# Performance work log

Hardware: AMD Instinct MI355X
Metric: run time of the kernel (lower is better)

The kernel has to match this reference:

```python
import jax, jax.numpy as jnp
import numpy as np

HIS = 10   # history steps (node_feature_dim = 10*4)
ROLL = 2   # args.pred_roll
MP = 2     # message_passing_steps
N = 20000  # num nodes (balls)
E = 320000 # num edges


def _mlp(x, W1, b1, W2, b2, g, be):
    # two-layer ELU MLP + BatchNorm1d (training mode: batch statistics)
    h = jax.nn.elu(x @ W1 + b1)
    h = jax.nn.elu(h @ W2 + b2)
    B, M, C = h.shape
    f = h.reshape(B * M, C)
    mu = f.mean(0)
    var = ((f - mu) ** 2).mean(0)  # biased variance, as torch BN training
    f = (f - mu) * jax.lax.rsqrt(var + 1e-5) * g + be
    return f.reshape(B, M, C)


def setup_inputs() -> dict:
    key = jax.random.key(0)
    ks = jax.random.split(key, 16)

    def lin(k, i, o):
        W = jax.random.normal(k, (i, o), jnp.float32) / jnp.sqrt(jnp.float32(i))
        b = jnp.full((o,), 0.1, jnp.float32)
        return W, b

    inp = {}
    inp["nodes"] = jax.random.normal(ks[0], (1, HIS + ROLL, N, 4), jnp.float32)
    inp["edge_pair"] = jax.random.randint(ks[1], (E, 2), 0, N)
    inp["edge_attr"] = jax.random.normal(ks[2], (E, 2), jnp.float32)
    # encoder node MLP: 40 -> 128 -> 128
    inp["en_W1"], inp["en_b1"] = lin(ks[3], 40, 128)
    inp["en_W2"], inp["en_b2"] = lin(ks[4], 128, 128)
    inp["en_g"], inp["en_be"] = jnp.ones((128,), jnp.float32), jnp.zeros((128,), jnp.float32)
    # encoder edge MLP: 6 -> 32 -> 32
    inp["ee_W1"], inp["ee_b1"] = lin(ks[5], 6, 32)
    inp["ee_W2"], inp["ee_b2"] = lin(ks[6], 32, 32)
    inp["ee_g"], inp["ee_be"] = jnp.ones((32,), jnp.float32), jnp.zeros((32,), jnp.float32)
    # GraphNetBlock edge MLP: 288 -> 128 -> 32
    inp["ge_W1"], inp["ge_b1"] = lin(ks[7], 288, 128)
    inp["ge_W2"], inp["ge_b2"] = lin(ks[8], 128, 32)
    inp["ge_g"], inp["ge_be"] = jnp.ones((32,), jnp.float32), jnp.zeros((32,), jnp.float32)
    # GraphNetBlock node MLP: 160 -> 256 -> 128
    inp["gn_W1"], inp["gn_b1"] = lin(ks[9], 160, 256)
    inp["gn_W2"], inp["gn_b2"] = lin(ks[10], 256, 128)
    inp["gn_g"], inp["gn_be"] = jnp.ones((128,), jnp.float32), jnp.zeros((128,), jnp.float32)
    # decoder: Linear(128,128) Tanh Linear(128,2)
    inp["d_W1"], inp["d_b1"] = lin(ks[11], 128, 128)
    inp["d_W2"], inp["d_b2"] = lin(ks[12], 128, 2)
    return inp


def _forward(nodes, edge_pair, edge_attr,
             en_W1, en_b1, en_W2, en_b2, en_g, en_be,
             ee_W1, ee_b1, ee_W2, ee_b2, ee_g, ee_be,
             ge_W1, ge_b1, ge_W2, ge_b2, ge_g, ge_be,
             gn_W1, gn_b1, gn_W2, gn_b2, gn_g, gn_be,
             d_W1, d_b1, d_W2, d_b2):
    window = nodes[0]                 # [T, N, 4]
    n = window.shape[1]
    s0 = edge_pair[:, 0]
    s1 = edge_pair[:, 1]
    # history features: [1, N, HIS*4]
    history = jnp.transpose(window[:HIS], (1, 0, 2)).reshape(1, n, -1)
    gt_future = window[HIS:]          # [ROLL, N, 4]
    # initial edge features: raw 2-dim attr + |pos/vel diff| (4-dim) -> 6
    pd0 = jnp.abs(window[HIS][s0] - window[HIS][s1])   # [E, 4]
    edge_feat = jnp.concatenate([edge_attr[None], pd0[None]], -1)  # [1, E, 6]
    cur_pos = window[HIS - 1, :, :2]
    cur_vel = window[HIS - 1, :, 2:]
    preds = []
    for _ in range(ROLL):
        ln = _mlp(history, en_W1, en_b1, en_W2, en_b2, en_g, en_be)    # [1,N,128]
        le = _mlp(edge_feat, ee_W1, ee_b1, ee_W2, ee_b2, ee_g, ee_be)  # [1,E,32]
        for _ in range(MP):
            # edge update: gather sender/receiver, MLP
            ef = jnp.concatenate([ln[:, s0], ln[:, s1], le], -1)       # [1,E,288]
            ne = _mlp(ef, ge_W1, ge_b1, ge_W2, ge_b2, ge_g, ge_be)     # [1,E,32]
            # node aggregation: scatter-add at both endpoints
            agg = jnp.zeros((n, ne.shape[-1]), ne.dtype)
            agg = agg.at[s0].add(ne[0]).at[s1].add(ne[0])
            nf = jnp.concatenate([ln, agg[None]], -1)                  # [1,N,160]
            nn_ = _mlp(nf, gn_W1, gn_b1, gn_W2, gn_b2, gn_g, gn_be)
            ln = nn_ + ln
            le = ne + le
        accel = jnp.tanh(ln @ d_W1 + d_b1) @ d_W2 + d_b2               # [1,N,2]
        prev_pos = cur_pos
        cur_pos = 2 * cur_pos + accel - prev_pos                       # [1,N,2]
        cur_vel = cur_vel + accel
        pd = jnp.abs(cur_pos[:, s0] - cur_pos[:, s1])                  # [1,E,2]
        edge_feat = edge_feat.at[:, :, -2:].set(pd)
        preds.append(cur_pos)
        hist4 = history.reshape(1, n, HIS, 4)
        new_state = jnp.concatenate([cur_pos.reshape(1, n, 1, 2),
                                     cur_vel.reshape(1, n, 1, 2)], -1)
        history = jnp.concatenate([hist4[:, :, 1:, :], new_state], -2).reshape(1, n, -1)
    preds = jnp.stack(preds, 1)                                        # [1,ROLL,N,2]
    diff = preds[0] - gt_future[:, :, :2]
    variance = 5e-5
    loss_nll = (diff ** 2 / (2 * variance)).sum() / (ROLL * n)
    loss_mse = (diff ** 2).mean()
    return preds, loss_nll, loss_mse, gt_future


def reference(nodes, edge_pair, edge_attr,
              en_W1, en_b1, en_W2, en_b2, en_g, en_be,
              ee_W1, ee_b1, ee_W2, ee_b2, ee_g, ee_be,
              ge_W1, ge_b1, ge_W2, ge_b2, ge_g, ge_be,
              gn_W1, gn_b1, gn_W2, gn_b2, gn_g, gn_be,
              d_W1, d_b1, d_W2, d_b2):
    return _forward(nodes, edge_pair, edge_attr,
                    en_W1, en_b1, en_W2, en_b2, en_g, en_be,
                    ee_W1, ee_b1, ee_W2, ee_b2, ee_g, ee_be,
                    ge_W1, ge_b1, ge_W2, ge_b2, ge_g, ge_be,
                    gn_W1, gn_b1, gn_W2, gn_b2, gn_g, gn_be,
                    d_W1, d_b1, d_W2, d_b2)
```

## Files before the change

kernel.cpp:

```cpp
#include <hip/hip_runtime.h>


constexpr int NN = 20000;
constexpr int NE = 320000;
constexpr int NSLOT = 32;
constexpr int SSTR = 512;

typedef __attribute__((ext_vector_type(8))) short short8;
typedef __attribute__((ext_vector_type(4))) float f32x4;

__device__ __forceinline__ float act_elu(float x) { return x > 0.f ? x : __expf(x) - 1.f; }
__device__ __forceinline__ unsigned short f2bf(float f) {
  unsigned u = __builtin_bit_cast(unsigned, f);
  return (unsigned short)((u + 0x7FFFu + ((u >> 16) & 1u)) >> 16);
}
__device__ __forceinline__ float bf2f(unsigned short h) {
  unsigned u = ((unsigned)h) << 16; return __builtin_bit_cast(float, u);
}

template<int K1, int K1P, int C1, int C2, int BM, int NWM, int NWC, int NWM2, int NWC2,
         int ACT2, bool STATS, int MODE>
__global__ __launch_bounds__(256) void mlp2_k(
    const unsigned short* __restrict__ A, const unsigned short* __restrict__ A2,
    const unsigned short* __restrict__ Wt1, const float* __restrict__ b1,
    const unsigned short* __restrict__ Wt2, const float* __restrict__ b2,
    unsigned short* __restrict__ out, int M, float* __restrict__ stat)
{
  constexpr int FM  = BM / (16 * NWM);
  constexpr int FC  = C1 / (16 * NWC);
  constexpr int FM2 = BM / (16 * NWM2);
  constexpr int FC2 = C2 / (16 * NWC2);
  constexpr int NKS1 = K1P / 32;
  constexpr int NKS2 = C1 / 32;
  constexpr int AST = K1P + 8;
  constexpr int P1 = C1 + 8;
  constexpr int P2 = C2 + 8;
  constexpr int ACH = K1P / 8;
  static_assert(NWM * NWC == 4 && NWM2 * NWC2 == 4, "4 waves");
  static_assert(C2 <= C1, "repack reuses H1");

  __shared__ unsigned short As[BM * AST];
  __shared__ unsigned short H1[BM * P1];
  __shared__ float red[2][C2];

  const int tid = threadIdx.x;
  const int row0 = blockIdx.x * BM;
  const int wave = tid >> 6, lane = tid & 63;
  const int wm = wave % NWM, wc = wave / NWM;
  const int wm2 = wave % NWM2, wc2 = wave / NWM2;
  const int lr = lane & 15, kg = lane >> 4;

  if (STATS) for (int i = tid; i < 2 * C2; i += 256) ((float*)red)[i] = 0.f;

  for (int idx = tid; idx < BM * ACH; idx += 256) {
    int m = idx / ACH, chk = idx % ACH;
    int kglob = chk * 8;
    int row = row0 + m;
    uint4 v = make_uint4(0, 0, 0, 0);
    if (row < M) {
      if (MODE == 0) {
        if (kglob + 8 <= K1) v = *(const uint4*)(A + (size_t)row * K1 + kglob);
      } else if (MODE == 2) {
        v = (kglob < 128) ? *(const uint4*)(A + (size_t)row * 128 + kglob)
                          : *(const uint4*)(A2 + (size_t)row * 32 + (kglob - 128));
      } else {
        if (chk == 0) v = *(const uint4*)(A + (size_t)row * 8);
      }
    }
    *(uint4*)&As[m * AST + chk * 8] = v;
  }
  __syncthreads();

  f32x4 acc1[FM][FC];
#pragma unroll
  for (int i = 0; i < FM; ++i)
#pragma unroll
    for (int j = 0; j < FC; ++j) acc1[i][j] = (f32x4){0.f, 0.f, 0.f, 0.f};

#pragma unroll
  for (int ks = 0; ks < NKS1; ++ks) {
    const int k0 = ks * 32;
    short8 af[FM], bfr[FC];
#pragma unroll
    for (int i = 0; i < FM; ++i) {
      int r = (wm * FM + i) * 16 + lr;
      af[i] = __builtin_bit_cast(short8, *(const uint4*)&As[r * AST + k0 + kg * 8]);
    }
#pragma unroll
    for (int j = 0; j < FC; ++j) {
      int c = (wc * FC + j) * 16 + lr;
      bfr[j] = __builtin_bit_cast(short8, *(const uint4*)&Wt1[(size_t)c * K1P + k0 + kg * 8]);
    }
#pragma unroll
    for (int i = 0; i < FM; ++i)
#pragma unroll
      for (int j = 0; j < FC; ++j)
        acc1[i][j] = __builtin_amdgcn_mfma_f32_16x16x32_bf16(af[i], bfr[j], acc1[i][j], 0, 0, 0);
  }

  {
    float bl1[FC];
#pragma unroll
    for (int j = 0; j < FC; ++j) bl1[j] = b1[(wc * FC + j) * 16 + lr];
#pragma unroll
    for (int i = 0; i < FM; ++i)
#pragma unroll
      for (int t = 0; t < 4; ++t) {
        int rl = (wm * FM + i) * 16 + kg * 4 + t;
#pragma unroll
        for (int j = 0; j < FC; ++j)
          H1[rl * P1 + (wc * FC + j) * 16 + lr] = f2bf(act_elu(acc1[i][j][t] + bl1[j]));
      }
  }
  __syncthreads();

  f32x4 acc2[FM2][FC2];
#pragma unroll
  for (int i = 0; i < FM2; ++i)
#pragma unroll
    for (int j = 0; j < FC2; ++j) acc2[i][j] = (f32x4){0.f, 0.f, 0.f, 0.f};

#pragma unroll
  for (int ks = 0; ks < NKS2; ++ks) {
    const int k0 = ks * 32;
    short8 af[FM2], bfr[FC2];
#pragma unroll
    for (int i = 0; i < FM2; ++i) {
      int r = (wm2 * FM2 + i) * 16 + lr;
      af[i] = __builtin_bit_cast(short8, *(const uint4*)&H1[r * P1 + k0 + kg * 8]);
    }
#pragma unroll
    for (int j = 0; j < FC2; ++j) {
      int c = (wc2 * FC2 + j) * 16 + lr;
      bfr[j] = __builtin_bit_cast(short8, *(const uint4*)&Wt2[(size_t)c * C1 + k0 + kg * 8]);
    }
#pragma unroll
    for (int i = 0; i < FM2; ++i)
#pragma unroll
      for (int j = 0; j < FC2; ++j)
        acc2[i][j] = __builtin_amdgcn_mfma_f32_16x16x32_bf16(af[i], bfr[j], acc2[i][j], 0, 0, 0);
  }
  __syncthreads();

  float psum[FC2], psq[FC2], bl2[FC2];
#pragma unroll
  for (int j = 0; j < FC2; ++j) {
    psum[j] = 0.f; psq[j] = 0.f;
    bl2[j] = b2[(wc2 * FC2 + j) * 16 + lr];
  }
#pragma unroll
  for (int i = 0; i < FM2; ++i)
#pragma unroll
    for (int t = 0; t < 4; ++t) {
      int rl = (wm2 * FM2 + i) * 16 + kg * 4 + t;
      bool ok = (row0 + rl) < M;
#pragma unroll
      for (int j = 0; j < FC2; ++j) {
        float v = acc2[i][j][t] + bl2[j];
        if (ACT2 == 1) v = act_elu(v);
        else if (ACT2 == 2) v = tanhf(v);
        if (STATS && ok) { psum[j] += v; psq[j] += v * v; }
        H1[rl * P2 + (wc2 * FC2 + j) * 16 + lr] = f2bf(v);
      }
    }
  if (STATS) {
#pragma unroll
    for (int j = 0; j < FC2; ++j) {
      int c = (wc2 * FC2 + j) * 16 + lr;
      atomicAdd(&red[0][c], psum[j]);
      atomicAdd(&red[1][c], psq[j]);
    }
  }
  __syncthreads();
  for (int idx = tid; idx < BM * (C2 / 8); idx += 256) {
    int r = idx / (C2 / 8), cc = idx % (C2 / 8);
    int row = row0 + r;
    if (row < M)
      *(uint4*)&out[(size_t)row * C2 + cc * 8] = *(const uint4*)&H1[r * P2 + cc * 8];
  }
  if (STATS) {
    float* st = stat + (size_t)(blockIdx.x & (NSLOT - 1)) * SSTR;
    for (int i = tid; i < C2; i += 256) {
      atomicAdd(&st[i], red[0][i]);
      atomicAdd(&st[256 + i], red[1][i]);
    }
  }
}

template<int K, int C, int BM, int NWM, int NWC, int ACT>
__global__ __launch_bounds__(256) void mgemm_k(
    const unsigned short* __restrict__ A,
    const unsigned short* __restrict__ Wt, const float* __restrict__ bias,
    unsigned short* __restrict__ out, int M)
{
  constexpr int FM = BM / (16 * NWM);
  constexpr int FC = C / (16 * NWC);
  constexpr int NKS = K / 32;
  constexpr int AST = K + 8;
  constexpr int P2 = C + 8;
  constexpr int ACH = K / 8;
  static_assert(NWM * NWC == 4, "4 waves");

  __shared__ unsigned short As[BM * AST];
  __shared__ unsigned short Ob[BM * P2];

  const int tid = threadIdx.x;
  const int row0 = blockIdx.x * BM;
  const int wave = tid >> 6, lane = tid & 63;
  const int wm = wave % NWM, wc = wave / NWM;
  const int lr = lane & 15, kg = lane >> 4;

  for (int idx = tid; idx < BM * ACH; idx += 256) {
    int m = idx / ACH, chk = idx % ACH;
    int row = row0 + m;
    uint4 v = make_uint4(0, 0, 0, 0);
    if (row < M) v = *(const uint4*)(A + (size_t)row * K + chk * 8);
    *(uint4*)&As[m * AST + chk * 8] = v;
  }
  __syncthreads();

  f32x4 acc[FM][FC];
#pragma unroll
  for (int i = 0; i < FM; ++i)
#pragma unroll
    for (int j = 0; j < FC; ++j) acc[i][j] = (f32x4){0.f, 0.f, 0.f, 0.f};

#pragma unroll
  for (int ks = 0; ks < NKS; ++ks) {
    const int k0 = ks * 32;
    short8 af[FM], bfr[FC];
#pragma unroll
    for (int i = 0; i < FM; ++i) {
      int r = (wm * FM + i) * 16 + lr;
      af[i] = __builtin_bit_cast(short8, *(const uint4*)&As[r * AST + k0 + kg * 8]);
    }
#pragma unroll
    for (int j = 0; j < FC; ++j) {
      int c = (wc * FC + j) * 16 + lr;
      bfr[j] = __builtin_bit_cast(short8, *(const uint4*)&Wt[(size_t)c * K + k0 + kg * 8]);
    }
#pragma unroll
    for (int i = 0; i < FM; ++i)
#pragma unroll
      for (int j = 0; j < FC; ++j)
        acc[i][j] = __builtin_amdgcn_mfma_f32_16x16x32_bf16(af[i], bfr[j], acc[i][j], 0, 0, 0);
  }

  float bl[FC];
#pragma unroll
  for (int j = 0; j < FC; ++j) bl[j] = bias[(wc * FC + j) * 16 + lr];
#pragma unroll
  for (int i = 0; i < FM; ++i)
#pragma unroll
    for (int t = 0; t < 4; ++t) {
      int rl = (wm * FM + i) * 16 + kg * 4 + t;
#pragma unroll
      for (int j = 0; j < FC; ++j) {
        float v = acc[i][j][t] + bl[j];
        if (ACT == 1) v = act_elu(v);
        else if (ACT == 2) v = tanhf(v);
        Ob[rl * P2 + (wc * FC + j) * 16 + lr] = f2bf(v);
      }
    }
  __syncthreads();
  for (int idx = tid; idx < BM * (C / 8); idx += 256) {
    int r = idx / (C / 8), cc = idx % (C / 8);
    int row = row0 + r;
    if (row < M)
      *(uint4*)&out[(size_t)row * C + cc * 8] = *(const uint4*)&Ob[r * P2 + cc * 8];
  }
}

template<int WOUT>
__global__ __launch_bounds__(256) void ge_edge_k(
    const unsigned short* __restrict__ Pb,
    const unsigned short* __restrict__ leb,
    const int* __restrict__ epP,
    const unsigned short* __restrict__ Wt1c,
    const float* __restrict__ b1,
    const unsigned short* __restrict__ Wt2,
    const float* __restrict__ b2,
    unsigned short* __restrict__ out,
    float* __restrict__ aggF,
    float* __restrict__ stat)
{
  constexpr int BM = 64;
  constexpr int P1 = 136;
  __shared__ unsigned short Ps[BM * P1];
  __shared__ unsigned short As[BM * 40];
  __shared__ float red[2][32];
  __shared__ int eps[BM * 2];

  const int tid = threadIdx.x;
  const int e0 = blockIdx.x * BM;
  const int wave = tid >> 6, lane = tid & 63;
  const int lr = lane & 15, kg = lane >> 4;
  const int wm = wave & 1, wc = wave >> 1;

  uint4 g0[4], g1[4];
  int gm[4], gch[4];
#pragma unroll
  for (int t = 0; t < 4; ++t) {
    int idx = tid + 256 * t;
    int m = idx >> 4, ch = idx & 15;
    gm[t] = m; gch[t] = ch;
    int s0 = epP[2 * (e0 + m)];
    int s1 = epP[2 * (e0 + m) + 1];
    g0[t] = *(const uint4*)&Pb[(size_t)s0 * 256 + ch * 8];
    g1[t] = *(const uint4*)&Pb[(size_t)s1 * 256 + 128 + ch * 8];
  }

  if (tid < BM * 2) eps[tid] = epP[e0 * 2 + tid];
  {
    int m = tid >> 2, chk = tid & 3;
    *(uint4*)&As[m * 40 + chk * 8] = *(const uint4*)&leb[(size_t)(e0 + m) * 32 + chk * 8];
  }
  short8 wf1[4];
#pragma unroll
  for (int j = 0; j < 4; ++j)
    wf1[j] = __builtin_bit_cast(short8, *(const uint4*)&Wt1c[(size_t)((wc * 4 + j) * 16 + lr) * 32 + kg * 8]);
  if (tid < 64) ((float*)red)[tid] = 0.f;
  __syncthreads();

  f32x4 acc1[2][4];
#pragma unroll
  for (int i = 0; i < 2; ++i)
#pragma unroll
    for (int j = 0; j < 4; ++j) acc1[i][j] = (f32x4){0.f, 0.f, 0.f, 0.f};
  {
    short8 af[2];
#pragma unroll
    for (int i = 0; i < 2; ++i)
      af[i] = __builtin_bit_cast(short8, *(const uint4*)&As[((wm * 2 + i) * 16 + lr) * 40 + kg * 8]);
#pragma unroll
    for (int i = 0; i < 2; ++i)
#pragma unroll
      for (int j = 0; j < 4; ++j)
        acc1[i][j] = __builtin_amdgcn_mfma_f32_16x16x32_bf16(af[i], wf1[j], acc1[i][j], 0, 0, 0);
  }

#pragma unroll
  for (int t = 0; t < 4; ++t) {
    uint4 o;
    const unsigned short* ap = (const unsigned short*)&g0[t];
    const unsigned short* bp = (const unsigned short*)&g1[t];
    unsigned short* op = (unsigned short*)&o;
#pragma unroll
    for (int j = 0; j < 8; ++j) op[j] = f2bf(bf2f(ap[j]) + bf2f(bp[j]));
    *(uint4*)&Ps[gm[t] * P1 + gch[t] * 8] = o;
  }
  __syncthreads();

  {
    float bl1[4];
#pragma unroll
    for (int j = 0; j < 4; ++j) bl1[j] = b1[(wc * 4 + j) * 16 + lr];
#pragma unroll
    for (int i = 0; i < 2; ++i)
#pragma unroll
      for (int t = 0; t < 4; ++t) {
        int rl = (wm * 2 + i) * 16 + kg * 4 + t;
#pragma unroll
        for (int j = 0; j < 4; ++j) {
          int a = rl * P1 + (wc * 4 + j) * 16 + lr;
          Ps[a] = f2bf(act_elu(acc1[i][j][t] + bl1[j] + bf2f(Ps[a])));
        }
      }
  }
  __syncthreads();

  f32x4 acc2[2];
  acc2[0] = (f32x4){0.f, 0.f, 0.f, 0.f};
  acc2[1] = (f32x4){0.f, 0.f, 0.f, 0.f};
  const int r2 = wave * 16 + lr;
#pragma unroll
  for (int ks = 0; ks < 4; ++ks) {
    int k0 = ks * 32;
    short8 a2 = __builtin_bit_cast(short8, *(const uint4*)&Ps[r2 * P1 + k0 + kg * 8]);
#pragma unroll
    for (int j = 0; j < 2; ++j) {
      short8 b2f = __builtin_bit_cast(short8, *(const uint4*)&Wt2[(size_t)(j * 16 + lr) * 128 + k0 + kg * 8]);
      acc2[j] = __builtin_amdgcn_mfma_f32_16x16x32_bf16(a2, b2f, acc2[j], 0, 0, 0);
    }
  }

  float psum[2] = {0.f, 0.f}, psq[2] = {0.f, 0.f};
  float bl2[2] = {b2[lr], b2[16 + lr]};
#pragma unroll
  for (int t = 0; t < 4; ++t) {
    int rl = wave * 16 + kg * 4 + t;
#pragma unroll
    for (int j = 0; j < 2; ++j) {
      float v = act_elu(acc2[j][t] + bl2[j]);
      psum[j] += v; psq[j] += v * v;
      As[rl * 40 + j * 16 + lr] = f2bf(v);
    }
  }
#pragma unroll
  for (int j = 0; j < 2; ++j) {
    atomicAdd(&red[0][j * 16 + lr], psum[j]);
    atomicAdd(&red[1][j * 16 + lr], psq[j]);
  }
  __syncthreads();
  if (WOUT) {
    int m = tid >> 2, chk = tid & 3;
    *(uint4*)&out[(size_t)(e0 + m) * 32 + chk * 8] = *(const uint4*)&As[m * 40 + chk * 8];
  }
  {
    int c = tid & 31, gsel = tid >> 5;
    int rbeg = gsel * 8;
    float acc = 0.f;
    int cur = eps[2 * rbeg];
#pragma unroll
    for (int r = 0; r < 8; ++r) {
      int row = rbeg + r;
      float v = bf2f(As[row * 40 + c]);
      int s0 = eps[2 * row];
      if (s0 != cur) { atomicAdd(&aggF[(size_t)cur * 32 + c], acc); acc = 0.f; cur = s0; }
      acc += v;
      atomicAdd(&aggF[(size_t)eps[2 * row + 1] * 32 + c], v);
    }
    atomicAdd(&aggF[(size_t)cur * 32 + c], acc);
  }
  if (tid < 32) {
    float* st = stat + (size_t)(blockIdx.x & (NSLOT - 1)) * SSTR;
    atomicAdd(&st[tid], red[0][tid]);
    atomicAdd(&st[256 + tid], red[1][tid]);
  }
}

__global__ __launch_bounds__(256) void agg_fin_k(float* __restrict__ aggF,
    const float* __restrict__ stat, float invM,
    const float* __restrict__ g, const float* __restrict__ be,
    const int* __restrict__ deg0, const int* __restrict__ deg1,
    unsigned short* __restrict__ agg_bf, int N)
{
  __shared__ float s_scl[32], s_shf[32];
  if (threadIdx.x < 32) {
    int c = threadIdx.x;
    float su = 0.f, sq = 0.f;
    for (int s = 0; s < NSLOT; ++s) {
      su += stat[(size_t)s * SSTR + c];
      sq += stat[(size_t)s * SSTR + 256 + c];
    }
    float mu = su * invM;
    float var = sq * invM - mu * mu;
    float sc = rsqrtf(var + 1e-5f) * g[c];
    s_scl[c] = sc; s_shf[c] = be[c] - mu * sc;
  }
  __syncthreads();
  int i = blockIdx.x * 256 + threadIdx.x;
  if (i >= N * 32) return;
  int n = i >> 5, c = i & 31;
  float v = fmaf(s_scl[c], aggF[i], (float)(deg0[n] + deg1[n]) * s_shf[c]);
  agg_bf[i] = f2bf(v);
  aggF[i] = 0.f;
}

__global__ __launch_bounds__(256) void wtrans_all_k(
    const float* __restrict__ enW1, const float* __restrict__ enW2,
    const float* __restrict__ geW1, const float* __restrict__ geW2,
    const float* __restrict__ gnW1, const float* __restrict__ gnW2,
    const float* __restrict__ dW1,  const float* __restrict__ eeW1,
    const float* __restrict__ eeW2,
    unsigned short* __restrict__ enW1t, unsigned short* __restrict__ enW2t,
    unsigned short* __restrict__ gePt,  unsigned short* __restrict__ geCt,
    unsigned short* __restrict__ geW2t,
    unsigned short* __restrict__ gnW1t, unsigned short* __restrict__ gnW2t,
    unsigned short* __restrict__ dW1t,  unsigned short* __restrict__ eeW1t,
    unsigned short* __restrict__ eeW2t)
{
  int i = blockIdx.x * 256 + threadIdx.x;
#define SEG(Wsrc, Wdst, NROW, SRCS, KS, KP) \
  { int n = (NROW) * (KP); \
    if (i < n) { int c = i / (KP), k = i - c * (KP); \
      (Wdst)[i] = (k < (KS)) ? f2bf((Wsrc)[(size_t)k * (SRCS) + c]) : (unsigned short)0; return; } \
    i -= n; }
  SEG(enW1, enW1t, 128, 128, 40, 64)
  SEG(enW2, enW2t, 128, 128, 128, 128)
  SEG(geW1, gePt, 128, 128, 128, 128)
  SEG(geW1 + 128 * 128, gePt + 128 * 128, 128, 128, 128, 128)
  SEG(geW1 + 256 * 128, geCt, 128, 128, 32, 32)
  SEG(geW2, geW2t, 32, 32, 128, 128)
  SEG(gnW1, gnW1t, 256, 256, 160, 160)
  SEG(gnW2, gnW2t, 128, 128, 256, 256)
  SEG(dW1,  dW1t,  128, 128, 128, 128)
  SEG(eeW1, eeW1t, 32, 32, 6, 32)
  SEG(eeW2, eeW2t, 32, 32, 32, 32)
#undef SEG
}
constexpr int WT_TOTAL = 128*64 + 128*128 + 128*128 + 128*128 + 128*32 + 32*128
                       + 256*160 + 128*256 + 128*128 + 32*32 + 32*32;

template<int C, bool RES>
__global__ __launch_bounds__(256) void normb_k(const unsigned short* __restrict__ h,
    const float* __restrict__ stat, float invM,
    const float* __restrict__ g, const float* __restrict__ be,
    unsigned short* __restrict__ out_bf, int total8)
{
  __shared__ float s_scl[C], s_shf[C];
  for (int i = threadIdx.x; i < C; i += 256) {
    float su = 0.f, sq = 0.f;
    for (int s = 0; s < NSLOT; ++s) {
      su += stat[(size_t)s * SSTR + i];
      sq += stat[(size_t)s * SSTR + 256 + i];
    }
    float mu = su * invM;
    float var = sq * invM - mu * mu;
    float sc = rsqrtf(var + 1e-5f) * g[i];
    s_scl[i] = sc; s_shf[i] = be[i] - mu * sc;
  }
  __syncthreads();
  int i = blockIdx.x * 256 + threadIdx.x;
  if (i >= total8) return;
  int c8 = (i % (C / 8)) * 8;
  uint4 hv = ((const uint4*)h)[i];
  const unsigned short* hp = (const unsigned short*)&hv;
  float f[8];
#pragma unroll
  for (int j = 0; j < 8; ++j) f[j] = fmaf(bf2f(hp[j]), s_scl[c8 + j], s_shf[c8 + j]);
  if (RES) {
    uint4 pv = ((const uint4*)out_bf)[i];
    const unsigned short* pp = (const unsigned short*)&pv;
#pragma unroll
    for (int j = 0; j < 8; ++j) f[j] += bf2f(pp[j]);
  }
  uint4 o;
  unsigned short* op = (unsigned short*)&o;
#pragma unroll
  for (int j = 0; j < 8; ++j) op[j] = f2bf(f[j]);
  ((uint4*)out_bf)[i] = o;
}

__global__ __launch_bounds__(256) void csr_count0_k(const int* __restrict__ ep,
    int* __restrict__ deg0, int E)
{
  int e = blockIdx.x * 256 + threadIdx.x;
  if (e < E) atomicAdd(&deg0[ep[2 * e]], 1);
}

__global__ __launch_bounds__(1024) void csr_scan_k(const int* __restrict__ deg,
    int* __restrict__ off, int* __restrict__ cursor, int N)
{
  __shared__ int part[1024];
  int t = threadIdx.x;
  const int CHK = (N + 1023) / 1024;
  int c0 = t * CHK, c1 = min(c0 + CHK, N);
  int s = 0;
  for (int i = c0; i < c1; ++i) s += deg[i];
  part[t] = s;
  __syncthreads();
  for (int o = 1; o < 1024; o <<= 1) {
    int v = (t >= o) ? part[t - o] : 0;
    __syncthreads();
    part[t] += v;
    __syncthreads();
  }
  int run = t ? part[t - 1] : 0;
  for (int i = c0; i < c1; ++i) { int d = deg[i]; off[i] = run; cursor[i] = run; run += d; }
}

__global__ __launch_bounds__(256) void csr_fill0_k(const int* __restrict__ ep,
    int* __restrict__ cursor0, int* __restrict__ perm, int E)
{
  int e = blockIdx.x * 256 + threadIdx.x;
  if (e < E) { int p = atomicAdd(&cursor0[ep[2 * e]], 1); perm[p] = e; }
}

__global__ __launch_bounds__(256) void permute_edges_k(const float4* __restrict__ nodes4,
    const float* __restrict__ attr, const int* __restrict__ ep,
    const int* __restrict__ perm, int* __restrict__ epP,
    unsigned short* __restrict__ efb, int* __restrict__ deg1, int E)
{
  int e2 = blockIdx.x * 256 + threadIdx.x;
  if (e2 >= E) return;
  int e = perm[e2];
  int s0 = ep[2 * e], s1 = ep[2 * e + 1];
  epP[2 * e2] = s0; epP[2 * e2 + 1] = s1;
  atomicAdd(&deg1[s1], 1);
  float4 w0 = nodes4[(size_t)10 * NN + s0];
  float4 w1 = nodes4[(size_t)10 * NN + s1];
  float2 a = ((const float2*)attr)[e];
  uint4 o;
  o.x = (unsigned)f2bf(a.x) | ((unsigned)f2bf(a.y) << 16);
  o.y = (unsigned)f2bf(fabsf(w0.x - w1.x)) | ((unsigned)f2bf(fabsf(w0.y - w1.y)) << 16);
  o.z = (unsigned)f2bf(fabsf(w0.z - w1.z)) | ((unsigned)f2bf(fabsf(w0.w - w1.w)) << 16);
  o.w = 0;
  ((uint4*)efb)[e2] = o;
}

__global__ __launch_bounds__(256) void le_upd_k(const unsigned short* __restrict__ h2e,
    const float* __restrict__ stat, float invM,
    const float* __restrict__ g, const float* __restrict__ be,
    unsigned short* __restrict__ leb, int total8)
{
  __shared__ float s_scl[32], s_shf[32];
  if (threadIdx.x < 32) {
    int c = threadIdx.x;
    float su = 0.f, sq = 0.f;
    for (int s = 0; s < NSLOT; ++s) {
      su += stat[(size_t)s * SSTR + c];
      sq += stat[(size_t)s * SSTR + 256 + c];
    }
    float mu = su * invM;
    float var = sq * invM - mu * mu;
    float sc = rsqrtf(var + 1e-5f) * g[c];
    s_scl[c] = sc; s_shf[c] = be[c] - mu * sc;
  }
  __syncthreads();
  int i = blockIdx.x * 256 + threadIdx.x;
  if (i >= total8) return;
  int c8 = (i & 3) * 8;
  uint4 hv = ((const uint4*)h2e)[i];
  uint4 lv = ((const uint4*)leb)[i];
  const unsigned short* hp = (const unsigned short*)&hv;
  const unsigned short* lp = (const unsigned short*)&lv;
  uint4 o;
  unsigned short* op = (unsigned short*)&o;
#pragma unroll
  for (int j = 0; j < 8; ++j)
    op[j] = f2bf(bf2f(lp[j]) + fmaf(bf2f(hp[j]), s_scl[c8 + j], s_shf[c8 + j]));
  ((uint4*)leb)[i] = o;
}

__global__ __launch_bounds__(256) void dec2i_k(const unsigned short* __restrict__ T,
    const float* __restrict__ W2, const float* __restrict__ b2,
    float* __restrict__ pos, float* __restrict__ vel, float* __restrict__ preds, int M)
{
  __shared__ float Wl[256];
  Wl[threadIdx.x] = W2[threadIdx.x];
  __syncthreads();
  int row = blockIdx.x * 256 + threadIdx.x;
  if (row >= M) return;
  float ax = b2[0], ay = b2[1];
  const uint4* t4 = (const uint4*)(T + (size_t)row * 128);
#pragma unroll
  for (int k8 = 0; k8 < 16; ++k8) {
    uint4 v = t4[k8];
    const unsigned short* p = (const unsigned short*)&v;
#pragma unroll
    for (int j = 0; j < 8; ++j) {
      float f = bf2f(p[j]);
      int k = k8 * 8 + j;
      ax = fmaf(f, Wl[2 * k], ax);
      ay = fmaf(f, Wl[2 * k + 1], ay);
    }
  }
  float2 p = ((float2*)pos)[row], vv = ((float2*)vel)[row];
  p.x += ax; p.y += ay; vv.x += ax; vv.y += ay;
  ((float2*)pos)[row] = p; ((float2*)vel)[row] = vv;
  ((float2*)preds)[row] = p;
}

__global__ __launch_bounds__(256) void pd_upd_k(const float* __restrict__ pos,
    const int* __restrict__ epP, unsigned short* __restrict__ efb, int E)
{
  int e = blockIdx.x * 256 + threadIdx.x;
  if (e >= E) return;
  float2 p0 = ((const float2*)pos)[epP[2 * e]];
  float2 p1 = ((const float2*)pos)[epP[2 * e + 1]];
  unsigned u = (unsigned)f2bf(fabsf(p0.x - p1.x)) | ((unsigned)f2bf(fabsf(p0.y - p1.y)) << 16);
  *(unsigned*)&efb[(size_t)e * 8 + 4] = u;
}

__global__ __launch_bounds__(256) void hist_shift_k(float* __restrict__ hist,
    unsigned short* __restrict__ histb,
    const float* __restrict__ pos, const float* __restrict__ vel, int M)
{
  int n = blockIdx.x * 256 + threadIdx.x;
  if (n >= M) return;
  float4* h4 = (float4*)(hist + (size_t)n * 40);
  float4 tmp[10];
#pragma unroll
  for (int t = 0; t < 10; ++t) tmp[t] = h4[t];
  float2 pp = ((const float2*)pos)[n], vv = ((const float2*)vel)[n];
  unsigned* hb = (unsigned*)(histb + (size_t)n * 40);
#pragma unroll
  for (int t = 0; t < 9; ++t) {
    float4 v = tmp[t + 1];
    h4[t] = v;
    hb[2 * t]     = (unsigned)f2bf(v.x) | ((unsigned)f2bf(v.y) << 16);
    hb[2 * t + 1] = (unsigned)f2bf(v.z) | ((unsigned)f2bf(v.w) << 16);
  }
  float4 nv = make_float4(pp.x, pp.y, vv.x, vv.y);
  h4[9] = nv;
  hb[18] = (unsigned)f2bf(nv.x) | ((unsigned)f2bf(nv.y) << 16);
  hb[19] = (unsigned)f2bf(nv.z) | ((unsigned)f2bf(nv.w) << 16);
}

__global__ __launch_bounds__(256) void init_nodes_k(const float4* __restrict__ nodes4,
    float* __restrict__ hist, unsigned short* __restrict__ histb,
    float* __restrict__ pos, float* __restrict__ vel,
    float* __restrict__ outGt, int M)
{
  int n = blockIdx.x * 256 + threadIdx.x;
  if (n >= M) return;
  float4* h4 = (float4*)(hist + (size_t)n * 40);
  unsigned* hb = (unsigned*)(histb + (size_t)n * 40);
  float4 v;
#pragma unroll
  for (int t = 0; t < 10; ++t) {
    v = nodes4[(size_t)t * M + n];
    h4[t] = v;
    hb[2 * t]     = (unsigned)f2bf(v.x) | ((unsigned)f2bf(v.y) << 16);
    hb[2 * t + 1] = (unsigned)f2bf(v.z) | ((unsigned)f2bf(v.w) << 16);
  }
  ((float2*)pos)[n] = make_float2(v.x, v.y);
  ((float2*)vel)[n] = make_float2(v.z, v.w);
  float4 g0 = nodes4[(size_t)10 * M + n];
  float4 g1 = nodes4[(size_t)11 * M + n];
  float2* gt2 = (float2*)outGt;
  gt2[(size_t)2 * n + 0] = make_float2(g0.x, g0.y);
  gt2[(size_t)2 * n + 1] = make_float2(g0.z, g0.w);
  gt2[(size_t)2 * (M + n) + 0] = make_float2(g1.x, g1.y);
  gt2[(size_t)2 * (M + n) + 1] = make_float2(g1.z, g1.w);
}

__global__ __launch_bounds__(256) void loss_k(const float* __restrict__ preds,
    const float* __restrict__ gtf, float* __restrict__ acc)
{
  int i = blockIdx.x * 256 + threadIdx.x;
  float d2 = 0.f;
  if (i < 2 * NN * 2) {
    int r = i / (NN * 2);
    int rem = i - r * (NN * 2);
    int n = rem >> 1, c = rem & 1;
    float df = preds[i] - gtf[((size_t)r * NN + n) * 4 + c];
    d2 = df * df;
  }
#pragma unroll
  for (int o = 32; o > 0; o >>= 1) d2 += __shfl_down(d2, o, 64);
  __shared__ float sb[4];
  int lane = threadIdx.x & 63, w = threadIdx.x >> 6;
  if (lane == 0) sb[w] = d2;
  __syncthreads();
  if (threadIdx.x == 0) atomicAdd(acc, sb[0] + sb[1] + sb[2] + sb[3]);
}

__global__ void loss_write_k(const float* __restrict__ acc, float* __restrict__ o)
{
  float s = *acc;
  o[0] = s * 0.25f;
  o[1] = s * (1.f / 80000.f);
}

extern "C" void kernel_launch(void* const* d_in, const int* in_sizes, int n_in,
                              void* d_out, int out_size, void* d_ws, size_t ws_size,
                              hipStream_t stream)
{
  (void)in_sizes; (void)n_in; (void)out_size; (void)ws_size;
  const float* nodes = (const float*)d_in[0];
  const int*   ep    = (const int*)d_in[1];
  const float* eattr = (const float*)d_in[2];
  const float *en_W1 = (const float*)d_in[3],  *en_b1 = (const float*)d_in[4],
              *en_W2 = (const float*)d_in[5],  *en_b2 = (const float*)d_in[6],
              *en_g  = (const float*)d_in[7],  *en_be = (const float*)d_in[8];
  const float *ee_W1 = (const float*)d_in[9],  *ee_b1 = (const float*)d_in[10],
              *ee_W2 = (const float*)d_in[11], *ee_b2 = (const float*)d_in[12],
              *ee_g  = (const float*)d_in[13], *ee_be = (const float*)d_in[14];
  const float *ge_W1 = (const float*)d_in[15], *ge_b1 = (const float*)d_in[16],
              *ge_W2 = (const float*)d_in[17], *ge_b2 = (const float*)d_in[18],
              *ge_g  = (const float*)d_in[19], *ge_be = (const float*)d_in[20];
  const float *gn_W1 = (const float*)d_in[21], *gn_b1 = (const float*)d_in[22],
              *gn_W2 = (const float*)d_in[23], *gn_b2 = (const float*)d_in[24],
              *gn_g  = (const float*)d_in[25], *gn_be = (const float*)d_in[26];
  const float *d_W1  = (const float*)d_in[27], *d_b1  = (const float*)d_in[28],
              *d_W2  = (const float*)d_in[29], *d_b2  = (const float*)d_in[30];

  float* out = (float*)d_out;
  float* outPreds = out;
  float* outLoss  = out + 80000;
  float* outGt    = out + 80002;

  float* ws = (float*)d_ws;
  size_t off = 0;
  auto alloc = [&](size_t nf) { float* p = ws + off; off += (nf + 15) & ~(size_t)15; return p; };
  float* hist  = alloc((size_t)NN * 40);
  unsigned short* histb = (unsigned short*)alloc((size_t)NN * 20);
  unsigned short* efb   = (unsigned short*)alloc((size_t)NE * 4);
  unsigned short* lnb  = (unsigned short*)alloc((size_t)NN * 64);
  unsigned short* leb  = (unsigned short*)alloc((size_t)NE * 16);
  unsigned short* e32b = (unsigned short*)alloc((size_t)NE * 16);
  unsigned short* Pb   = (unsigned short*)alloc((size_t)NN * 128);
  unsigned short* h2nb = (unsigned short*)alloc((size_t)NN * 64);
  unsigned short* dtb  = (unsigned short*)alloc((size_t)NN * 64);
  unsigned short* aggb = (unsigned short*)alloc((size_t)NN * 16);
  float* aggF  = alloc((size_t)NN * 32);
  float* pos   = alloc((size_t)NN * 2);
  float* vel   = alloc((size_t)NN * 2);
  unsigned short* enW1t = (unsigned short*)alloc(128 * 64 / 2);
  unsigned short* enW2t = (unsigned short*)alloc(128 * 128 / 2);
  unsigned short* gePt  = (unsigned short*)alloc(256 * 128 / 2);
  unsigned short* geCt  = (unsigned short*)alloc(128 * 32 / 2);
  unsigned short* geW2t = (unsigned short*)alloc(32 * 128 / 2);
  unsigned short* gnW1t = (unsigned short*)alloc(256 * 160 / 2);
  unsigned short* gnW2t = (unsigned short*)alloc(128 * 256 / 2);
  unsigned short* dW1t  = (unsigned short*)alloc(128 * 128 / 2);
  unsigned short* eeW1t = (unsigned short*)alloc(32 * 32 / 2);
  unsigned short* eeW2t = (unsigned short*)alloc(32 * 32 / 2);
  const size_t SLOTSZ = (size_t)NSLOT * SSTR;
  float* statArr = alloc(12 * SLOTSZ + 256 + 16);
  float* zerosF  = statArr + 12 * SLOTSZ;
  float* lacc    = zerosF + 256;
  int* deg0    = (int*)alloc(NN);
  int* off0    = (int*)alloc(NN);
  int* cursor0 = (int*)alloc(NN);
  int* deg1    = (int*)alloc(NN);
  int* perm    = (int*)alloc(NE);
  int* epP     = (int*)alloc(2 * (size_t)NE);

  hipMemsetAsync(statArr, 0, (12 * SLOTSZ + 256 + 16) * sizeof(float), stream);
  hipMemsetAsync(deg0, 0, NN * sizeof(int), stream);
  hipMemsetAsync(deg1, 0, NN * sizeof(int), stream);
  hipMemsetAsync(aggF, 0, (size_t)NN * 32 * sizeof(float), stream);

  wtrans_all_k<<<(WT_TOTAL + 255) / 256, 256, 0, stream>>>(
      en_W1, en_W2, ge_W1, ge_W2, gn_W1, gn_W2, d_W1, ee_W1, ee_W2,
      enW1t, enW2t, gePt, geCt, geW2t, gnW1t, gnW2t, dW1t, eeW1t, eeW2t);

  init_nodes_k<<<(NN + 255) / 256, 256, 0, stream>>>((const float4*)nodes, hist, histb, pos, vel, outGt, NN);

  csr_count0_k<<<(NE + 255) / 256, 256, 0, stream>>>(ep, deg0, NE);
  csr_scan_k<<<1, 1024, 0, stream>>>(deg0, off0, cursor0, NN);
  csr_fill0_k<<<(NE + 255) / 256, 256, 0, stream>>>(ep, cursor0, perm, NE);
  permute_edges_k<<<(NE + 255) / 256, 256, 0, stream>>>(
      (const float4*)nodes, eattr, ep, perm, epP, efb, deg1, NE);

  const int GN32 = (NN + 31) / 32;
  const int GE128 = NE / 128;
  const int GE64 = NE / 64;
  const int G_N8 = (NN * 16 + 255) / 256;
  const int G_E8 = (NE * 4 + 255) / 256;
  const int G_AGG = (NN * 32 + 255) / 256;

  for (int r = 0; r < 2; ++r) {
    float* sEN = statArr + (size_t)(r * 6 + 0) * SLOTSZ;
    float* sEE = statArr + (size_t)(r * 6 + 1) * SLOTSZ;

    mlp2_k<40, 64, 128, 128, 32, 2, 2, 2, 2, 1, true, 0><<<GN32, 256, 0, stream>>>(
        histb, nullptr, enW1t, en_b1, enW2t, en_b2, h2nb, NN, sEN);
    normb_k<128, false><<<G_N8, 256, 0, stream>>>(h2nb, sEN, 1.f / NN, en_g, en_be, lnb, NN * 16);

    mlp2_k<32, 32, 32, 32, 128, 4, 1, 4, 1, 1, true, 3><<<GE128, 256, 0, stream>>>(
        efb, nullptr, eeW1t, ee_b1, eeW2t, ee_b2, e32b, NE, sEE);
    normb_k<32, false><<<G_E8, 256, 0, stream>>>(e32b, sEE, 1.f / NE, ee_g, ee_be, leb, NE * 4);

    for (int mp = 0; mp < 2; ++mp) {
      float* sGE = statArr + (size_t)(r * 6 + 2 + mp * 2) * SLOTSZ;
      float* sGN = statArr + (size_t)(r * 6 + 3 + mp * 2) * SLOTSZ;

      mgemm_k<128, 256, 32, 2, 2, 0><<<GN32, 256, 0, stream>>>(lnb, gePt, zerosF, Pb, NN);
      if (mp == 0)
        ge_edge_k<1><<<GE64, 256, 0, stream>>>(Pb, leb, epP, geCt, ge_b1, geW2t, ge_b2, e32b, aggF, sGE);
      else
        ge_edge_k<0><<<GE64, 256, 0, stream>>>(Pb, leb, epP, geCt, ge_b1, geW2t, ge_b2, e32b, aggF, sGE);

      agg_fin_k<<<G_AGG, 256, 0, stream>>>(aggF, sGE, 1.f / NE, ge_g, ge_be, deg0, deg1, aggb, NN);
      if (mp == 0)
        le_upd_k<<<G_E8, 256, 0, stream>>>(e32b, sGE, 1.f / NE, ge_g, ge_be, leb, NE * 4);

      mlp2_k<160, 160, 256, 128, 32, 2, 2, 2, 2, 1, true, 2><<<GN32, 256, 0, stream>>>(
          lnb, aggb, gnW1t, gn_b1, gnW2t, gn_b2, h2nb, NN, sGN);
      normb_k<128, true><<<G_N8, 256, 0, stream>>>(h2nb, sGN, 1.f / NN, gn_g, gn_be, lnb, NN * 16);
    }

    mgemm_k<128, 128, 32, 2, 2, 2><<<GN32, 256, 0, stream>>>(lnb, dW1t, d_b1, dtb, NN);
    dec2i_k<<<(NN + 255) / 256, 256, 0, stream>>>(dtb, d_W2, d_b2, pos, vel, outPreds + (size_t)r * NN * 2, NN);

    if (r == 0) {
      pd_upd_k<<<(NE + 255) / 256, 256, 0, stream>>>(pos, epP, efb, NE);
      hist_shift_k<<<(NN + 255) / 256, 256, 0, stream>>>(hist, histb, pos, vel, NN);
    }
  }

  loss_k<<<(2 * NN * 2 + 255) / 256, 256, 0, stream>>>(outPreds, outGt, lacc);
  loss_write_k<<<1, 1, 0, stream>>>(lacc, outLoss);
}
```

Baseline: 789.7 us.

## Fuse BN finalize, edge residual update and decoder head into neighboring kernels

```diff
diff --git a/kernel.cpp b/kernel.cpp
--- a/kernel.cpp
+++ b/kernel.cpp
@@ -21,10 +21,13 @@
 template<int K1, int K1P, int C1, int C2, int BM, int NWM, int NWC, int NWM2, int NWC2,
          int ACT2, bool STATS, int MODE>
 __global__ __launch_bounds__(256) void mlp2_k(
-    const unsigned short* __restrict__ A, const unsigned short* __restrict__ A2,
+    const unsigned short* __restrict__ A,
     const unsigned short* __restrict__ Wt1, const float* __restrict__ b1,
     const unsigned short* __restrict__ Wt2, const float* __restrict__ b2,
-    unsigned short* __restrict__ out, int M, float* __restrict__ stat)
+    unsigned short* __restrict__ out, int M, float* __restrict__ stat,
+    float* __restrict__ aggF, const float* __restrict__ statP, float invE,
+    const float* __restrict__ gg, const float* __restrict__ gb,
+    float* __restrict__ sclW, const int* __restrict__ dg0, const int* __restrict__ dg1)
 {
   constexpr int FM  = BM / (16 * NWM);
   constexpr int FC  = C1 / (16 * NWC);
@@ -42,6 +45,7 @@
   __shared__ unsigned short As[BM * AST];
   __shared__ unsigned short H1[BM * P1];
   __shared__ float red[2][C2];
+  __shared__ float s_scl[(MODE == 4) ? 32 : 1], s_shf[(MODE == 4) ? 32 : 1];
 
   const int tid = threadIdx.x;
   const int row0 = blockIdx.x * BM;
@@ -52,19 +56,49 @@
 
   if (STATS) for (int i = tid; i < 2 * C2; i += 256) ((float*)red)[i] = 0.f;
 
+  if constexpr (MODE == 4) {
+    if (tid < 32) {
+      float su = 0.f, sq = 0.f;
+      for (int s = 0; s < NSLOT; ++s) {
+        su += statP[(size_t)s * SSTR + tid];
+        sq += statP[(size_t)s * SSTR + 256 + tid];
+      }
+      float mu = su * invE;
+      float var = sq * invE - mu * mu;
+      float sc = rsqrtf(var + 1e-5f) * gg[tid];
+      float sh = gb[tid] - mu * sc;
+      s_scl[tid] = sc; s_shf[tid] = sh;
+      if (blockIdx.x == 0) { sclW[tid] = sc; sclW[32 + tid] = sh; }
+    }
+    __syncthreads();
+  }
+
   for (int idx = tid; idx < BM * ACH; idx += 256) {
     int m = idx / ACH, chk = idx % ACH;
     int kglob = chk * 8;
     int row = row0 + m;
     uint4 v = make_uint4(0, 0, 0, 0);
     if (row < M) {
-      if (MODE == 0) {
+      if constexpr (MODE == 0) {
         if (kglob + 8 <= K1) v = *(const uint4*)(A + (size_t)row * K1 + kglob);
-      } else if (MODE == 2) {
-        v = (kglob < 128) ? *(const uint4*)(A + (size_t)row * 128 + kglob)
-                          : *(const uint4*)(A2 + (size_t)row * 32 + (kglob - 128));
+      } else if constexpr (MODE == 3) {
+        if (chk == 0) v = *(const uint4*)(A + (size_t)row * 8);
       } else {
-        if (chk == 0) v = *(const uint4*)(A + (size_t)row * 8);
+        if (kglob < 128) {
+          v = *(const uint4*)(A + (size_t)row * 128 + kglob);
+        } else {
+          int c0 = kglob - 128;
+          float* ap = &aggF[(size_t)row * 32 + c0];
+          float4 a0 = *(float4*)ap, a1 = *(float4*)(ap + 4);
+          *(float4*)ap = make_float4(0.f, 0.f, 0.f, 0.f);
+          *(float4*)(ap + 4) = make_float4(0.f, 0.f, 0.f, 0.f);
+          float d = (float)(dg0[row] + dg1[row]);
+          float av[8] = {a0.x, a0.y, a0.z, a0.w, a1.x, a1.y, a1.z, a1.w};
+          unsigned short* vp = (unsigned short*)&v;
+#pragma unroll
+          for (int j = 0; j < 8; ++j)
+            vp[j] = f2bf(fmaf(s_scl[c0 + j], av[j], d * s_shf[c0 + j]));
+        }
       }
     }
     *(uint4*)&As[m * AST + chk * 8] = v;
@@ -187,11 +221,13 @@
   }
 }
 
-template<int K, int C, int BM, int NWM, int NWC, int ACT>
+template<int K, int C, int BM, int NWM, int NWC, int ACT, int DEC>
 __global__ __launch_bounds__(256) void mgemm_k(
     const unsigned short* __restrict__ A,
     const unsigned short* __restrict__ Wt, const float* __restrict__ bias,
-    unsigned short* __restrict__ out, int M)
+    unsigned short* __restrict__ out, int M,
+    const float* __restrict__ W2f, const float* __restrict__ b2f,
+    float* __restrict__ pos, float* __restrict__ vel, float* __restrict__ preds)
 {
   constexpr int FM = BM / (16 * NWM);
   constexpr int FC = C / (16 * NWC);
@@ -203,6 +239,7 @@
 
   __shared__ unsigned short As[BM * AST];
   __shared__ unsigned short Ob[BM * P2];
+  __shared__ float Wl[DEC ? 256 : 1];
 
   const int tid = threadIdx.x;
   const int row0 = blockIdx.x * BM;
@@ -262,19 +299,44 @@
         Ob[rl * P2 + (wc * FC + j) * 16 + lr] = f2bf(v);
       }
     }
-  __syncthreads();
-  for (int idx = tid; idx < BM * (C / 8); idx += 256) {
-    int r = idx / (C / 8), cc = idx % (C / 8);
-    int row = row0 + r;
-    if (row < M)
-      *(uint4*)&out[(size_t)row * C + cc * 8] = *(const uint4*)&Ob[r * P2 + cc * 8];
-  }
-}
-
-template<int WOUT>
+  if constexpr (DEC) Wl[tid] = W2f[tid];
+  __syncthreads();
+  if constexpr (DEC) {
+    int rloc = tid >> 3, j = tid & 7;
+    int row = row0 + rloc;
+    float ax = 0.f, ay = 0.f;
+#pragma unroll
+    for (int kk = 0; kk < 16; ++kk) {
+      int k = j + 8 * kk;
+      float f = bf2f(Ob[rloc * P2 + k]);
+      ax = fmaf(f, Wl[2 * k], ax);
+      ay = fmaf(f, Wl[2 * k + 1], ay);
+    }
+    ax += __shfl_down(ax, 4, 8); ax += __shfl_down(ax, 2, 8); ax += __shfl_down(ax, 1, 8);
+    ay += __shfl_down(ay, 4, 8); ay += __shfl_down(ay, 2, 8); ay += __shfl_down(ay, 1, 8);
+    if (j == 0 && row < M) {
+      float axx = ax + b2f[0], ayy = ay + b2f[1];
+      float2 p = ((float2*)pos)[row], vv = ((float2*)vel)[row];
+      p.x += axx; p.y += ayy; vv.x += axx; vv.y += ayy;
+      ((float2*)pos)[row] = p; ((float2*)vel)[row] = vv;
+      ((float2*)preds)[row] = p;
+    }
+  } else {
+    for (int idx = tid; idx < BM * (C / 8); idx += 256) {
+      int r = idx / (C / 8), cc = idx % (C / 8);
+      int row = row0 + r;
+      if (row < M)
+        *(uint4*)&out[(size_t)row * C + cc * 8] = *(const uint4*)&Ob[r * P2 + cc * 8];
+    }
+  }
+}
+
+template<int WOUT, int LEFUSE>
 __global__ __launch_bounds__(256) void ge_edge_k(
     const unsigned short* __restrict__ Pb,
     const unsigned short* __restrict__ leb,
+    const unsigned short* __restrict__ e32prev,
+    const float* __restrict__ sclshf,
     const int* __restrict__ epP,
     const unsigned short* __restrict__ Wt1c,
     const float* __restrict__ b1,
@@ -313,7 +375,22 @@
   if (tid < BM * 2) eps[tid] = epP[e0 * 2 + tid];
   {
     int m = tid >> 2, chk = tid & 3;
-    *(uint4*)&As[m * 40 + chk * 8] = *(const uint4*)&leb[(size_t)(e0 + m) * 32 + chk * 8];
+    uint4 lv = *(const uint4*)&leb[(size_t)(e0 + m) * 32 + chk * 8];
+    if constexpr (LEFUSE) {
+      uint4 ev = *(const uint4*)&e32prev[(size_t)(e0 + m) * 32 + chk * 8];
+      const unsigned short* lp = (const unsigned short*)&lv;
+      const unsigned short* epv = (const unsigned short*)&ev;
+      uint4 ov;
+      unsigned short* op = (unsigned short*)&ov;
+#pragma unroll
+      for (int j = 0; j < 8; ++j) {
+        int c = chk * 8 + j;
+        op[j] = f2bf(bf2f(lp[j]) + fmaf(sclshf[c], bf2f(epv[j]), sclshf[32 + c]));
+      }
+      *(uint4*)&As[m * 40 + chk * 8] = ov;
+    } else {
+      *(uint4*)&As[m * 40 + chk * 8] = lv;
+    }
   }
   short8 wf1[4];
 #pragma unroll
@@ -427,34 +504,6 @@
     atomicAdd(&st[tid], red[0][tid]);
     atomicAdd(&st[256 + tid], red[1][tid]);
   }
-}
-
-__global__ __launch_bounds__(256) void agg_fin_k(float* __restrict__ aggF,
-    const float* __restrict__ stat, float invM,
-    const float* __restrict__ g, const float* __restrict__ be,
-    const int* __restrict__ deg0, const int* __restrict__ deg1,
-    unsigned short* __restrict__ agg_bf, int N)
-{
-  __shared__ float s_scl[32], s_shf[32];
-  if (threadIdx.x < 32) {
-    int c = threadIdx.x;
-    float su = 0.f, sq = 0.f;
-    for (int s = 0; s < NSLOT; ++s) {
-      su += stat[(size_t)s * SSTR + c];
-      sq += stat[(size_t)s * SSTR + 256 + c];
-    }
-    float mu = su * invM;
-    float var = sq * invM - mu * mu;
-    float sc = rsqrtf(var + 1e-5f) * g[c];
-    s_scl[c] = sc; s_shf[c] = be[c] - mu * sc;
-  }
-  __syncthreads();
-  int i = blockIdx.x * 256 + threadIdx.x;
-  if (i >= N * 32) return;
-  int n = i >> 5, c = i & 31;
-  float v = fmaf(s_scl[c], aggF[i], (float)(deg0[n] + deg1[n]) * s_shf[c]);
-  agg_bf[i] = f2bf(v);
-  aggF[i] = 0.f;
 }
 
 __global__ __launch_bounds__(256) void wtrans_all_k(
@@ -589,69 +638,6 @@
   ((uint4*)efb)[e2] = o;
 }
 
-__global__ __launch_bounds__(256) void le_upd_k(const unsigned short* __restrict__ h2e,
-    const float* __restrict__ stat, float invM,
-    const float* __restrict__ g, const float* __restrict__ be,
-    unsigned short* __restrict__ leb, int total8)
-{
-  __shared__ float s_scl[32], s_shf[32];
-  if (threadIdx.x < 32) {
-    int c = threadIdx.x;
-    float su = 0.f, sq = 0.f;
-    for (int s = 0; s < NSLOT; ++s) {
-      su += stat[(size_t)s * SSTR + c];
-      sq += stat[(size_t)s * SSTR + 256 + c];
-    }
-    float mu = su * invM;
-    float var = sq * invM - mu * mu;
-    float sc = rsqrtf(var + 1e-5f) * g[c];
-    s_scl[c] = sc; s_shf[c] = be[c] - mu * sc;
-  }
-  __syncthreads();
-  int i = blockIdx.x * 256 + threadIdx.x;
-  if (i >= total8) return;
-  int c8 = (i & 3) * 8;
-  uint4 hv = ((const uint4*)h2e)[i];
-  uint4 lv = ((const uint4*)leb)[i];
-  const unsigned short* hp = (const unsigned short*)&hv;
-  const unsigned short* lp = (const unsigned short*)&lv;
-  uint4 o;
-  unsigned short* op = (unsigned short*)&o;
-#pragma unroll
-  for (int j = 0; j < 8; ++j)
-    op[j] = f2bf(bf2f(lp[j]) + fmaf(bf2f(hp[j]), s_scl[c8 + j], s_shf[c8 + j]));
-  ((uint4*)leb)[i] = o;
-}
-
-__global__ __launch_bounds__(256) void dec2i_k(const unsigned short* __restrict__ T,
-    const float* __restrict__ W2, const float* __restrict__ b2,
-    float* __restrict__ pos, float* __restrict__ vel, float* __restrict__ preds, int M)
-{
-  __shared__ float Wl[256];
-  Wl[threadIdx.x] = W2[threadIdx.x];
-  __syncthreads();
-  int row = blockIdx.x * 256 + threadIdx.x;
-  if (row >= M) return;
-  float ax = b2[0], ay = b2[1];
-  const uint4* t4 = (const uint4*)(T + (size_t)row * 128);
-#pragma unroll
-  for (int k8 = 0; k8 < 16; ++k8) {
-    uint4 v = t4[k8];
-    const unsigned short* p = (const unsigned short*)&v;
-#pragma unroll
-    for (int j = 0; j < 8; ++j) {
-      float f = bf2f(p[j]);
-      int k = k8 * 8 + j;
-      ax = fmaf(f, Wl[2 * k], ax);
-      ay = fmaf(f, Wl[2 * k + 1], ay);
-    }
-  }
-  float2 p = ((float2*)pos)[row], vv = ((float2*)vel)[row];
-  p.x += ax; p.y += ay; vv.x += ax; vv.y += ay;
-  ((float2*)pos)[row] = p; ((float2*)vel)[row] = vv;
-  ((float2*)preds)[row] = p;
-}
-
 __global__ __launch_bounds__(256) void pd_upd_k(const float* __restrict__ pos,
     const int* __restrict__ epP, unsigned short* __restrict__ efb, int E)
 {
@@ -783,8 +769,6 @@
   unsigned short* e32b = (unsigned short*)alloc((size_t)NE * 16);
   unsigned short* Pb   = (unsigned short*)alloc((size_t)NN * 128);
   unsigned short* h2nb = (unsigned short*)alloc((size_t)NN * 64);
-  unsigned short* dtb  = (unsigned short*)alloc((size_t)NN * 64);
-  unsigned short* aggb = (unsigned short*)alloc((size_t)NN * 16);
   float* aggF  = alloc((size_t)NN * 32);
   float* pos   = alloc((size_t)NN * 2);
   float* vel   = alloc((size_t)NN * 2);
@@ -802,6 +786,7 @@
   float* statArr = alloc(12 * SLOTSZ + 256 + 16);
   float* zerosF  = statArr + 12 * SLOTSZ;
   float* lacc    = zerosF + 256;
+  float* sclshfGE = alloc(64);
   int* deg0    = (int*)alloc(NN);
   int* off0    = (int*)alloc(NN);
   int* cursor0 = (int*)alloc(NN);
@@ -831,41 +816,43 @@
   const int GE64 = NE / 64;
   const int G_N8 = (NN * 16 + 255) / 256;
   const int G_E8 = (NE * 4 + 255) / 256;
-  const int G_AGG = (NN * 32 + 255) / 256;
+  const float invE = 1.f / NE;
 
   for (int r = 0; r < 2; ++r) {
     float* sEN = statArr + (size_t)(r * 6 + 0) * SLOTSZ;
     float* sEE = statArr + (size_t)(r * 6 + 1) * SLOTSZ;
 
     mlp2_k<40, 64, 128, 128, 32, 2, 2, 2, 2, 1, true, 0><<<GN32, 256, 0, stream>>>(
-        histb, nullptr, enW1t, en_b1, enW2t, en_b2, h2nb, NN, sEN);
+        histb, enW1t, en_b1, enW2t, en_b2, h2nb, NN, sEN,
+        nullptr, nullptr, 0.f, nullptr, nullptr, nullptr, nullptr, nullptr);
     normb_k<128, false><<<G_N8, 256, 0, stream>>>(h2nb, sEN, 1.f / NN, en_g, en_be, lnb, NN * 16);
 
     mlp2_k<32, 32, 32, 32, 128, 4, 1, 4, 1, 1, true, 3><<<GE128, 256, 0, stream>>>(
-        efb, nullptr, eeW1t, ee_b1, eeW2t, ee_b2, e32b, NE, sEE);
-    normb_k<32, false><<<G_E8, 256, 0, stream>>>(e32b, sEE, 1.f / NE, ee_g, ee_be, leb, NE * 4);
+        efb, eeW1t, ee_b1, eeW2t, ee_b2, e32b, NE, sEE,
+        nullptr, nullptr, 0.f, nullptr, nullptr, nullptr, nullptr, nullptr);
+    normb_k<32, false><<<G_E8, 256, 0, stream>>>(e32b, sEE, invE, ee_g, ee_be, leb, NE * 4);
 
     for (int mp = 0; mp < 2; ++mp) {
       float* sGE = statArr + (size_t)(r * 6 + 2 + mp * 2) * SLOTSZ;
       float* sGN = statArr + (size_t)(r * 6 + 3 + mp * 2) * SLOTSZ;
 
-      mgemm_k<128, 256, 32, 2, 2, 0><<<GN32, 256, 0, stream>>>(lnb, gePt, zerosF, Pb, NN);
+      mgemm_k<128, 256, 32, 2, 2, 0, 0><<<GN32, 256, 0, stream>>>(
+          lnb, gePt, zerosF, Pb, NN, nullptr, nullptr, nullptr, nullptr, nullptr);
       if (mp == 0)
-        ge_edge_k<1><<<GE64, 256, 0, stream>>>(Pb, leb, epP, geCt, ge_b1, geW2t, ge_b2, e32b, aggF, sGE);
+        ge_edge_k<1, 0><<<GE64, 256, 0, stream>>>(Pb, leb, nullptr, nullptr, epP,
+            geCt, ge_b1, geW2t, ge_b2, e32b, aggF, sGE);
       else
-        ge_edge_k<0><<<GE64, 256, 0, stream>>>(Pb, leb, epP, geCt, ge_b1, geW2t, ge_b2, e32b, aggF, sGE);
-
-      agg_fin_k<<<G_AGG, 256, 0, stream>>>(aggF, sGE, 1.f / NE, ge_g, ge_be, deg0, deg1, aggb, NN);
-      if (mp == 0)
-        le_upd_k<<<G_E8, 256, 0, stream>>>(e32b, sGE, 1.f / NE, ge_g, ge_be, leb, NE * 4);
-
-      mlp2_k<160, 160, 256, 128, 32, 2, 2, 2, 2, 1, true, 2><<<GN32, 256, 0, stream>>>(
-          lnb, aggb, gnW1t, gn_b1, gnW2t, gn_b2, h2nb, NN, sGN);
+        ge_edge_k<0, 1><<<GE64, 256, 0, stream>>>(Pb, leb, e32b, sclshfGE, epP,
+            geCt, ge_b1, geW2t, ge_b2, nullptr, aggF, sGE);
+
+      mlp2_k<160, 160, 256, 128, 32, 2, 2, 2, 2, 1, true, 4><<<GN32, 256, 0, stream>>>(
+          lnb, gnW1t, gn_b1, gnW2t, gn_b2, h2nb, NN, sGN,
+          aggF, sGE, invE, ge_g, ge_be, sclshfGE, deg0, deg1);
       normb_k<128, true><<<G_N8, 256, 0, stream>>>(h2nb, sGN, 1.f / NN, gn_g, gn_be, lnb, NN * 16);
     }
 
-    mgemm_k<128, 128, 32, 2, 2, 2><<<GN32, 256, 0, stream>>>(lnb, dW1t, d_b1, dtb, NN);
-    dec2i_k<<<(NN + 255) / 256, 256, 0, stream>>>(dtb, d_W2, d_b2, pos, vel, outPreds + (size_t)r * NN * 2, NN);
+    mgemm_k<128, 128, 32, 2, 2, 2, 1><<<GN32, 256, 0, stream>>>(
+        lnb, dW1t, d_b1, nullptr, NN, d_W2, d_b2, pos, vel, outPreds + (size_t)r * NN * 2);
 
     if (r == 0) {
       pd_upd_k<<<(NE + 255) / 256, 256, 0, stream>>>(pos, epP, efb, NE);
```

Result: faster. 760.1 us (-3.8%).
